# Kernel optimization log

Measured on AMD Instinct MI355X. Metric: run time of the kernel, lower is better.

Reference implementation:

```python
import jax, jax.numpy as jnp
import numpy as np
from jax import lax

EPS = 1e-8
DN = ('NCHW', 'OIHW', 'NCHW')


def setup_inputs() -> dict:
    key = jax.random.key(0)
    k1, k2 = jax.random.split(key)
    inputs = jax.random.normal(k1, (16, 3, 512, 512), dtype=jnp.float32)
    template = jax.random.normal(k2, (16, 3, 21, 21), dtype=jnp.float32)
    return {"inputs": inputs, "template": template}


def _normalize_template(template):
    # Z-normalize each (batch, channel) plane independently, then divide by
    # patch element count (matches NCC.__init__).
    B, C, th, tw = template.shape
    t = template.reshape(B, C, th * tw)
    t = t - jnp.mean(t, axis=-1, keepdims=True)
    t = t / (jnp.std(t, axis=-1, keepdims=True) + EPS)  # ddof=0 == unbiased=False
    return t.reshape(B, C, th, tw) / (th * tw)


def reference(inputs, template):
    B, C, H, W = inputs.shape
    th, tw = template.shape[2], template.shape[3]
    nt = _normalize_template(template)

    # Per-(b,c) depthwise cross-correlation (the grouped conv with eye-masked
    # weights is exactly a depthwise conv with per-sample filters).
    x = inputs.reshape(1, B * C, H, W)
    w = nt.reshape(B * C, 1, th, tw)
    res = lax.conv_general_dilated(x, w, (1, 1), 'VALID',
                                   dimension_numbers=DN,
                                   feature_group_count=B * C)
    res = res.reshape(B, C, res.shape[2], res.shape[3])  # (B,C,Hout,Wout)

    # Local (patch) std per channel via box filter (shared across batch).
    box = jnp.full((C, 1, th, tw), 1.0 / (th * tw), dtype=inputs.dtype)
    mean = lax.conv_general_dilated(inputs, box, (1, 1), 'VALID',
                                    dimension_numbers=DN, feature_group_count=C)
    mean_sq = lax.conv_general_dilated(inputs * inputs, box, (1, 1), 'VALID',
                                       dimension_numbers=DN, feature_group_count=C)
    std = jnp.sqrt(mean_sq - mean * mean + EPS)

    return res / (std + EPS)
```

## Files before the change

kernel.cpp:

```cpp
#include <hip/hip_runtime.h>
#include <math.h>

typedef __attribute__((ext_vector_type(8)))  short short8;
typedef __attribute__((ext_vector_type(16))) float f32x16;

#define NPLANE 48
#define H 512
#define W 512
#define TH 21
#define OH 492
#define OW 492
#define EPSF 1e-8f

#define STRIDE 168
#define SEG_ROWS 84

#define BONES_HOFF (4128768u / 2)

__device__ inline unsigned short f2bf(float f) {
    unsigned u = __float_as_uint(f);
    return (unsigned short)((u + 0x7FFFu + ((u >> 16) & 1u)) >> 16);
}
__device__ inline unsigned cvtpk(float lo, float hi) {
    unsigned r;
    asm("v_cvt_pk_bf16_f32 %0, %1, %2" : "=v"(r) : "v"(lo), "v"(hi));
    return r;
}
__device__ inline float unpk_lo(unsigned p) { return __uint_as_float(p << 16); }
__device__ inline float unpk_hi(unsigned p) {
    return __uint_as_float(p & 0xffff0000u);
}

__global__ void build_b_kernel(const float* __restrict__ tpl,
                               unsigned short* __restrict__ ws16) {
    __shared__ float sm[2];
    const int plane = blockIdx.x;
    const float* t = tpl + plane * 441;
    const int tid = threadIdx.x;
    if (tid < 64) {
        float s = 0.f, s2 = 0.f;
        for (int k = tid; k < 441; k += 64) {
            float x = t[k];
            s += x; s2 += x * x;
        }
#pragma unroll
        for (int o = 32; o >= 1; o >>= 1) {
            s  += __shfl_down(s, o);
            s2 += __shfl_down(s2, o);
        }
        if (tid == 0) {
            float mean = s / 441.f;
            float var = fmaxf(s2 / 441.f - mean * mean, 0.f);
            sm[0] = mean;
            sm[1] = 1.f / ((sqrtf(var) + EPSF) * 441.f);
        }
    }
    __syncthreads();
    const float mean = sm[0], scale = sm[1];

    unsigned short* bc = ws16 + (size_t)plane * 43008;
    for (int i = tid; i < 43008; i += 256) {
        int j = i & 7, lane = (i >> 3) & 63, s = (i >> 9) & 3, u = i >> 11;
        int k = ((lane >> 5) << 3) + j, n = lane & 31;
        int v = 16 * s + k - n;
        float val = (v >= 0 && v < TH) ? (t[u * 21 + v] - mean) * scale : 0.f;
        bc[i] = f2bf(val);
    }
    if (plane == 0) {
        unsigned short* bo = ws16 + BONES_HOFF;
        const unsigned short one = f2bf(1.f);
        for (int i = tid; i < 2048; i += 256) {
            int j = i & 7, lane = (i >> 3) & 63, s = (i >> 9) & 3;
            int k = ((lane >> 5) << 3) + j, n = lane & 31;
            int v = 16 * s + k - n;
            bo[i] = (v >= 0 && v < TH) ? one : (unsigned short)0;
        }
    }
}

__global__ __launch_bounds__(256, 3) void ncc_fused_kernel(
    const float* __restrict__ in, const unsigned short* __restrict__ ws16,
    float* __restrict__ out) {
    __shared__ short seg[SEG_ROWS * STRIDE];
    __shared__ short vbuf[64 * STRIDE];

    const int plane = blockIdx.z;
    const int x0 = blockIdx.x * 128;
    const int y0 = blockIdx.y * 64;
    const int tid = threadIdx.x;
    const int lane = tid & 63;
    const int tr = (tid >> 6) & 1;
    const int tc = tid >> 7;
    const float* src = in + (size_t)plane * H * W;

    for (int i = tid; i < SEG_ROWS * 20; i += 256) {
        int row = i / 20, s8 = i - row * 20;
        int gy = y0 + row, gx = x0 + s8 * 8;
        if (gy < H && gx + 7 < W) {
            float4 a = *(const float4*)(src + gy * W + gx);
            float4 b = *(const float4*)(src + gy * W + gx + 4);
            uint4 v;
            v.x = cvtpk(a.x, a.y);
            v.y = cvtpk(a.z, a.w);
            v.z = cvtpk(b.x, b.y);
            v.w = cvtpk(b.z, b.w);
            *(uint4*)&seg[row * STRIDE + s8 * 8] = v;
        } else {
            short8 val;
#pragma unroll
            for (int e = 0; e < 8; ++e) {
                float xv = (gy < H && gx + e < W) ? src[gy * W + gx + e] : 0.f;
                val[e] = (short)f2bf(xv);
            }
            *(short8*)&seg[row * STRIDE + s8 * 8] = val;
        }
    }
    __syncthreads();

    const int m = lane & 31;
    const int half = lane >> 5;
    const int abase = (tr * 32 + m) * STRIDE + tc * 64 + half * 8;
    const unsigned short* bc = ws16 + (size_t)plane * 43008 + lane * 8;

    f32x16 acc[2];
#pragma unroll
    for (int t = 0; t < 2; ++t)
#pragma unroll
        for (int e = 0; e < 16; ++e) acc[t][e] = 0.f;

    auto corr_step = [&](int u, short8* bf) {
        short8 af[6];
#pragma unroll
        for (int g = 0; g < 6; ++g)
            af[g] = *(const short8*)&seg[abase + u * STRIDE + g * 16];
#pragma unroll
        for (int s = 0; s < 4; ++s)
#pragma unroll
            for (int t = 0; t < 2; ++t)
                acc[t] = __builtin_amdgcn_mfma_f32_32x32x16_bf16(
                    af[2 * t + s], bf[s], acc[t], 0, 0, 0);
    };

    auto bload = [&](short8* dst, int u) {
#pragma unroll
        for (int s = 0; s < 4; ++s)
            dst[s] = *(const short8*)(bc + (u * 4 + s) * 512);
    };

    short8 b0[4], b1[4], b2[4];
    bload(b0, 0); bload(b1, 1); bload(b2, 2);
    for (int u = 0; u < TH; u += 3) {
        corr_step(u, b0);
        bload(b0, (u + 3 < TH) ? u + 3 : 0);
        corr_step(u + 1, b1);
        bload(b1, (u + 4 < TH) ? u + 4 : 0);
        corr_step(u + 2, b2);
        bload(b2, (u + 5 < TH) ? u + 5 : 0);
    }

    const unsigned short* bo16 = ws16 + BONES_HOFF + lane * 8;
    short8 bones[4];
#pragma unroll
    for (int s = 0; s < 4; ++s)
        bones[s] = *(const short8*)(bo16 + s * 512);

    auto vpass = [&](bool sq) {
        if (tid < 160) {
            const int hr = (tid >= 80) ? 32 : 0;
            const int c2 = (tid % 80) * 2;
            float s0 = 0.f, s1 = 0.f;
#pragma unroll
            for (int r = 0; r < 20; ++r) {
                unsigned p = *(const unsigned*)&seg[(hr + r) * STRIDE + c2];
                float a = unpk_lo(p), b = unpk_hi(p);
                if (sq) { s0 = fmaf(a, a, s0); s1 = fmaf(b, b, s1); }
                else    { s0 += a; s1 += b; }
            }
#pragma unroll
            for (int yy = 0; yy < 32; yy += 8) {
                unsigned pin[8], pout[8];
#pragma unroll
                for (int r = 0; r < 8; ++r) {
                    pin[r]  = *(const unsigned*)
                        &seg[(hr + yy + r + 20) * STRIDE + c2];
                    pout[r] = *(const unsigned*)
                        &seg[(hr + yy + r) * STRIDE + c2];
                }
#pragma unroll
                for (int r = 0; r < 8; ++r) {
                    float a = unpk_lo(pin[r]), b = unpk_hi(pin[r]);
                    if (sq) { s0 = fmaf(a, a, s0); s1 = fmaf(b, b, s1); }
                    else    { s0 += a; s1 += b; }
                    *(unsigned*)&vbuf[(hr + yy + r) * STRIDE + c2] =
                        cvtpk(s0, s1);
                    float c = unpk_lo(pout[r]), d = unpk_hi(pout[r]);
                    if (sq) { s0 = fmaf(-c, c, s0); s1 = fmaf(-d, d, s1); }
                    else    { s0 -= c; s1 -= d; }
                }
            }
        }
    };

    vpass(false);
    __syncthreads();

    f32x16 aS[2];
#pragma unroll
    for (int t = 0; t < 2; ++t)
#pragma unroll
        for (int e = 0; e < 16; ++e) aS[t][e] = 0.f;
#pragma unroll
    for (int s = 0; s < 4; ++s)
#pragma unroll
        for (int t = 0; t < 2; ++t) {
            short8 vf = *(const short8*)&vbuf[abase + (2 * t + s) * 16];
            aS[t] = __builtin_amdgcn_mfma_f32_32x32x16_bf16(vf, bones[s],
                                                            aS[t], 0, 0, 0);
        }
    __syncthreads();

    vpass(true);
    __syncthreads();

    f32x16 aQ[2];
#pragma unroll
    for (int t = 0; t < 2; ++t)
#pragma unroll
        for (int e = 0; e < 16; ++e) aQ[t][e] = 0.f;
#pragma unroll
    for (int s = 0; s < 4; ++s)
#pragma unroll
        for (int t = 0; t < 2; ++t) {
            short8 qf = *(const short8*)&vbuf[abase + (2 * t + s) * 16];
            aQ[t] = __builtin_amdgcn_mfma_f32_32x32x16_bf16(qf, bones[s],
                                                            aQ[t], 0, 0, 0);
        }

    const float invn = 1.f / 441.f;
    float* outp = out + (size_t)plane * OH * OW;
#pragma unroll
    for (int t = 0; t < 2; ++t) {
        float vout[16];
#pragma unroll
        for (int r = 0; r < 16; ++r) {
            float mean = aS[t][r] * invn;
            float msq = aQ[t][r] * invn;
            float var = fmaf(-mean, mean, msq) + EPSF;
            vout[r] = acc[t][r] * __builtin_amdgcn_rsqf(var);
        }
        const int gx = x0 + tc * 64 + t * 32 + m;
        if (gx < OW) {
#pragma unroll
            for (int r = 0; r < 16; ++r) {
                int gy = y0 + tr * 32 + (r & 3) + ((r >> 2) << 3) + half * 4;
                if (gy < OH)
                    outp[(size_t)gy * OW + gx] = vout[r];
            }
        }
    }
}

extern "C" void kernel_launch(void* const* d_in, const int* in_sizes, int n_in,
                              void* d_out, int out_size, void* d_ws,
                              size_t ws_size, hipStream_t stream) {
    const float* inputs = (const float*)d_in[0];
    const float* tmpl = (const float*)d_in[1];
    float* out = (float*)d_out;
    unsigned short* ws16 = (unsigned short*)d_ws;

    build_b_kernel<<<NPLANE, 256, 0, stream>>>(tmpl, ws16);
    ncc_fused_kernel<<<dim3(4, 8, NPLANE), 256, 0, stream>>>(inputs, ws16, out);
}
```

Baseline: 161.7 us.

## Overlap correlation MFMA with box-filter vertical passes across wave groups

Splits the workgroup so one half of the waves (tc==0) runs the template correlation while the other half computes the vertical running sum, then swaps roles for the squared-sum pass. The vertical pass now uses 80 threads each covering all 64 rows, keeping a 20-row register history instead of re-reading outgoing rows from LDS. The goal is to hide the scalar LDS-bound box-filter work behind MFMA work rather than running them serially. In exchange, each correlation runs on only half the waves at a time, and the 20-entry history adds register pressure.

```diff
diff --git a/kernel.cpp b/kernel.cpp
--- a/kernel.cpp
+++ b/kernel.cpp
@@ -115,93 +115,88 @@
             *(short8*)&seg[row * STRIDE + s8 * 8] = val;
         }
     }
-    __syncthreads();
 
     const int m = lane & 31;
     const int half = lane >> 5;
     const int abase = (tr * 32 + m) * STRIDE + tc * 64 + half * 8;
     const unsigned short* bc = ws16 + (size_t)plane * 43008 + lane * 8;
 
-    f32x16 acc[2];
-#pragma unroll
-    for (int t = 0; t < 2; ++t)
-#pragma unroll
-        for (int e = 0; e < 16; ++e) acc[t][e] = 0.f;
-
-    auto corr_step = [&](int u, short8* bf) {
-        short8 af[6];
-#pragma unroll
-        for (int g = 0; g < 6; ++g)
-            af[g] = *(const short8*)&seg[abase + u * STRIDE + g * 16];
-#pragma unroll
-        for (int s = 0; s < 4; ++s)
-#pragma unroll
-            for (int t = 0; t < 2; ++t)
-                acc[t] = __builtin_amdgcn_mfma_f32_32x32x16_bf16(
-                    af[2 * t + s], bf[s], acc[t], 0, 0, 0);
-    };
-
-    auto bload = [&](short8* dst, int u) {
-#pragma unroll
-        for (int s = 0; s < 4; ++s)
-            dst[s] = *(const short8*)(bc + (u * 4 + s) * 512);
-    };
-
-    short8 b0[4], b1[4], b2[4];
-    bload(b0, 0); bload(b1, 1); bload(b2, 2);
-    for (int u = 0; u < TH; u += 3) {
-        corr_step(u, b0);
-        bload(b0, (u + 3 < TH) ? u + 3 : 0);
-        corr_step(u + 1, b1);
-        bload(b1, (u + 4 < TH) ? u + 4 : 0);
-        corr_step(u + 2, b2);
-        bload(b2, (u + 5 < TH) ? u + 5 : 0);
-    }
-
     const unsigned short* bo16 = ws16 + BONES_HOFF + lane * 8;
     short8 bones[4];
 #pragma unroll
     for (int s = 0; s < 4; ++s)
         bones[s] = *(const short8*)(bo16 + s * 512);
 
-    auto vpass = [&](bool sq) {
-        if (tid < 160) {
-            const int hr = (tid >= 80) ? 32 : 0;
-            const int c2 = (tid % 80) * 2;
-            float s0 = 0.f, s1 = 0.f;
-#pragma unroll
-            for (int r = 0; r < 20; ++r) {
-                unsigned p = *(const unsigned*)&seg[(hr + r) * STRIDE + c2];
-                float a = unpk_lo(p), b = unpk_hi(p);
-                if (sq) { s0 = fmaf(a, a, s0); s1 = fmaf(b, b, s1); }
-                else    { s0 += a; s1 += b; }
-            }
-#pragma unroll
-            for (int yy = 0; yy < 32; yy += 8) {
-                unsigned pin[8], pout[8];
-#pragma unroll
-                for (int r = 0; r < 8; ++r) {
-                    pin[r]  = *(const unsigned*)
-                        &seg[(hr + yy + r + 20) * STRIDE + c2];
-                    pout[r] = *(const unsigned*)
-                        &seg[(hr + yy + r) * STRIDE + c2];
-                }
-#pragma unroll
-                for (int r = 0; r < 8; ++r) {
-                    float a = unpk_lo(pin[r]), b = unpk_hi(pin[r]);
-                    if (sq) { s0 = fmaf(a, a, s0); s1 = fmaf(b, b, s1); }
-                    else    { s0 += a; s1 += b; }
-                    *(unsigned*)&vbuf[(hr + yy + r) * STRIDE + c2] =
-                        cvtpk(s0, s1);
-                    float c = unpk_lo(pout[r]), d = unpk_hi(pout[r]);
-                    if (sq) { s0 = fmaf(-c, c, s0); s1 = fmaf(-d, d, s1); }
-                    else    { s0 -= c; s1 -= d; }
-                }
-            }
+    f32x16 acc[2];
+
+    auto corr_all = [&]() {
+#pragma unroll
+        for (int t = 0; t < 2; ++t)
+#pragma unroll
+            for (int e = 0; e < 16; ++e) acc[t][e] = 0.f;
+        auto corr_step = [&](int u, short8* bf) {
+            short8 af[6];
+#pragma unroll
+            for (int g = 0; g < 6; ++g)
+                af[g] = *(const short8*)&seg[abase + u * STRIDE + g * 16];
+#pragma unroll
+            for (int s = 0; s < 4; ++s)
+#pragma unroll
+                for (int t = 0; t < 2; ++t)
+                    acc[t] = __builtin_amdgcn_mfma_f32_32x32x16_bf16(
+                        af[2 * t + s], bf[s], acc[t], 0, 0, 0);
+        };
+        auto bload = [&](short8* dst, int u) {
+#pragma unroll
+            for (int s = 0; s < 4; ++s)
+                dst[s] = *(const short8*)(bc + (u * 4 + s) * 512);
+        };
+        short8 b0[4], b1[4], b2[4];
+        bload(b0, 0); bload(b1, 1); bload(b2, 2);
+        for (int u = 0; u < TH; u += 3) {
+            corr_step(u, b0);
+            bload(b0, (u + 3 < TH) ? u + 3 : 0);
+            corr_step(u + 1, b1);
+            bload(b1, (u + 4 < TH) ? u + 4 : 0);
+            corr_step(u + 2, b2);
+            bload(b2, (u + 5 < TH) ? u + 5 : 0);
         }
     };
 
-    vpass(false);
+    auto vpass_roll = [&](bool sq, int cp) {
+        const int c2 = cp * 2;
+        float s0 = 0.f, s1 = 0.f;
+        unsigned hist[20];
+#pragma unroll
+        for (int r = 0; r < 20; ++r) {
+            unsigned p = *(const unsigned*)&seg[r * STRIDE + c2];
+            hist[r] = p;
+            float a = unpk_lo(p), b = unpk_hi(p);
+            if (sq) { s0 = fmaf(a, a, s0); s1 = fmaf(b, b, s1); }
+            else    { s0 += a; s1 += b; }
+        }
+#pragma unroll
+        for (int y = 0; y < 64; ++y) {
+            unsigned p = *(const unsigned*)&seg[(y + 20) * STRIDE + c2];
+            float a = unpk_lo(p), b = unpk_hi(p);
+            if (sq) { s0 = fmaf(a, a, s0); s1 = fmaf(b, b, s1); }
+            else    { s0 += a; s1 += b; }
+            *(unsigned*)&vbuf[y * STRIDE + c2] = cvtpk(s0, s1);
+            unsigned q = hist[y % 20];
+            float c = unpk_lo(q), d = unpk_hi(q);
+            if (sq) { s0 = fmaf(-c, c, s0); s1 = fmaf(-d, d, s1); }
+            else    { s0 -= c; s1 -= d; }
+            hist[y % 20] = p;
+        }
+    };
+
+    __syncthreads();
+
+    if (tc == 0) {
+        corr_all();
+    } else if (tid - 128 < 80) {
+        vpass_roll(false, tid - 128);
+    }
     __syncthreads();
 
     f32x16 aS[2];
@@ -219,7 +214,11 @@
         }
     __syncthreads();
 
-    vpass(true);
+    if (tc == 1) {
+        corr_all();
+    } else if (tid < 80) {
+        vpass_roll(true, tid);
+    }
     __syncthreads();
 
     f32x16 aQ[2];
```

Result: no change. 163.7 us (+1.2%).
